# Performance work log

Hardware: AMD Instinct MI355X
Metric: run time of the kernel (lower is better)

Reference implementation:

```python
import jax, jax.numpy as jnp
import numpy as np
from jax import lax
from jax.scipy.special import logsumexp

B, T, L, K = 4, 512, 96, 64  # batch, sample_size, num_label, segment_max_len
W = K - 1                    # number of non-zero-start segment lengths considered
NEG = -1e30


def setup_inputs() -> dict:
    key = jax.random.key(0)
    k1, k2 = jax.random.split(key)
    segment_score = jax.random.normal(k1, (B, T, T, L), dtype=jnp.float32)
    transitions = jax.random.uniform(k2, (L + 1, L), dtype=jnp.float32)  # row L = BOS
    return {"segment_score": segment_score, "transitions": transitions}


def _log_z(segment_score, transitions):
    dtype = segment_score.dtype
    trans = transitions[:L]   # [Lp, Lc]
    bos = transitions[L]      # [Lc]
    # NOTE: original code stores exp(...) (not log) for frame 0 -- preserved faithfully.
    alpha0 = jnp.zeros((B, T, L), dtype)
    alpha0 = alpha0.at[:, 0, :].set(jnp.exp(segment_score[:, 0, 0, :] + bos[None, :]))

    w = jnp.arange(1, W + 1, dtype=dtype)  # weight (j+1) per window slot
    jidx = jnp.arange(W)

    def step(alpha, t):
        # scores of all segments ending at frame t: [B, T(start), L]
        seg_t = lax.dynamic_slice(segment_score, (0, 0, t, 0), (B, T, 1, L))[:, :, 0, :]
        base = jnp.maximum(t - W, 0)
        m = jnp.minimum(t, W)  # number of valid non-zero-start entries
        # window slot j: start frame = base+1+j, prev alpha frame = base+j, weight = j+1
        seg_win = lax.dynamic_slice(seg_t, (0, base + 1, 0), (B, W, L))      # [B,W,Lc]
        alpha_win = lax.dynamic_slice(alpha, (0, base, 0), (B, W, L))        # [B,W,Lp]
        total = (alpha_win[:, :, :, None]
                 + (seg_win * w[None, :, None])[:, :, None, :]
                 + (trans[None, :, :] * w[:, None, None])[None, :, :, :])    # [B,W,Lp,Lc]
        total = jnp.where(jidx[None, :, None, None] < m, total, NEG)
        # zero-start segment (only when t+1 <= K i.e. t <= W)
        tlen = (t + 1).astype(dtype)
        z = seg_t[:, 0, :] * tlen + bos[None, :] * tlen                       # [B,Lc]
        z = jnp.where(t <= W, z, NEG)
        cat = jnp.concatenate([total.reshape(B, W * L, L), z[:, None, :]], axis=1)
        new = logsumexp(cat, axis=1)                                          # [B,Lc]
        alpha = lax.dynamic_update_slice(alpha, new[:, None, :], (0, t, 0))
        return alpha, None

    alpha, _ = lax.scan(step, alpha0, jnp.arange(1, T))
    return logsumexp(alpha[:, T - 1, :], axis=1)  # [B]


def reference(segment_score, transitions):
    return _log_z(segment_score, transitions)
```

## Files before the change

### kernel.cpp

```cpp
#include <hip/hip_runtime.h>


#define Tn 512
#define Ln 96
#define HL 48
#define LSQ (Ln * Ln)
#define Wn 63
#define KCH 8
#define NROLE 32
#define NEGINF (-1e30f)
#define SENT 0x7FC00000u

#define AGENT __HIP_MEMORY_SCOPE_AGENT
#define WG __HIP_MEMORY_SCOPE_WORKGROUP
#define RLX __ATOMIC_RELAXED
#define LDSF() asm volatile("s_waitcnt lgkmcnt(0)" ::: "memory")
#define CBAR() asm volatile("" ::: "memory")
#define SIDX(b, i, t) ((((size_t)(b) * Tn + (i)) * Tn + (t)) * Ln)

typedef unsigned long long u64;
typedef unsigned int u32;
typedef unsigned short u16;

__device__ __forceinline__ float wsumred(float v) {
#pragma unroll
  for (int m = 32; m >= 1; m >>= 1) v += __shfl_xor(v, m, 64);
  return v;
}
__device__ __forceinline__ u64 pack2(float lo, float hi) {
  return (u64)__float_as_uint(lo) | ((u64)__float_as_uint(hi) << 32);
}
__device__ __forceinline__ u16 tobf16(float x) {
  return (u16)((__float_as_uint(x) + 0x8000u) >> 16);
}
__device__ __forceinline__ float wavemax48(float v) {
  int x;
  x = __builtin_amdgcn_update_dpp(__float_as_int(v), __float_as_int(v), 0xB1,
                                  0xF, 0xF, false);
  v = fmaxf(v, __int_as_float(x));
  x = __builtin_amdgcn_update_dpp(__float_as_int(v), __float_as_int(v), 0x4E,
                                  0xF, 0xF, false);
  v = fmaxf(v, __int_as_float(x));
  x = __builtin_amdgcn_update_dpp(__float_as_int(v), __float_as_int(v), 0x141,
                                  0xF, 0xF, false);
  v = fmaxf(v, __int_as_float(x));
  x = __builtin_amdgcn_update_dpp(__float_as_int(v), __float_as_int(v), 0x140,
                                  0xF, 0xF, false);
  v = fmaxf(v, __int_as_float(x));
  float r0 = __int_as_float(__builtin_amdgcn_readlane(__float_as_int(v), 0));
  float r1 = __int_as_float(__builtin_amdgcn_readlane(__float_as_int(v), 16));
  float r2 = __int_as_float(__builtin_amdgcn_readlane(__float_as_int(v), 32));
  float r3 = __int_as_float(__builtin_amdgcn_readlane(__float_as_int(v), 48));
  return fmaxf(fmaxf(r0, r1), fmaxf(r2, r3));
}
__device__ __forceinline__ float comb(float Slo, float Shi, float C0, float C1,
                                      float wseg) {
  const float Cm = fmaxf(C0, C1);
  return Cm + wseg + __logf(__expf(C0 - Cm) * Slo + __expf(C1 - Cm) * Shi);
}

#define MV1(SRC, RR, SLO, SHI)                                       \
  float SLO, SHI;                                                    \
  {                                                                  \
    const float4* A4 = (const float4*)(SRC);                         \
    float a0 = 0, a1 = 0, a2 = 0, a3 = 0;                            \
    _Pragma("unroll") for (int q = 0; q < 12; ++q) {                 \
      float4 a = A4[q];                                              \
      a0 = fmaf(a.x, RR[4 * q + 0], a0);                             \
      a1 = fmaf(a.y, RR[4 * q + 1], a1);                             \
      a2 = fmaf(a.z, RR[4 * q + 2], a2);                             \
      a3 = fmaf(a.w, RR[4 * q + 3], a3);                             \
    }                                                                \
    SLO = (a0 + a1) + (a2 + a3);                                     \
    float b0 = 0, b1 = 0, b2 = 0, b3 = 0;                            \
    _Pragma("unroll") for (int q = 12; q < 24; ++q) {                \
      float4 a = A4[q];                                              \
      b0 = fmaf(a.x, RR[4 * q + 0], b0);                             \
      b1 = fmaf(a.y, RR[4 * q + 1], b1);                             \
      b2 = fmaf(a.z, RR[4 * q + 2], b2);                             \
      b3 = fmaf(a.w, RR[4 * q + 3], b3);                             \
    }                                                                \
    SHI = (b0 + b1) + (b2 + b3);                                     \
  }

#define MVB(SRC, RR, SLO, SHI)                                               \
  float SLO, SHI;                                                            \
  {                                                                          \
    const uint4* A4 = (const uint4*)(SRC);                                   \
    float a0 = 0, a1 = 0, a2 = 0, a3 = 0;                                    \
    _Pragma("unroll") for (int q = 0; q < 6; ++q) {                          \
      uint4 a = A4[q];                                                       \
      a0 = fmaf(__uint_as_float(a.x << 16), RR[8 * q + 0], a0);              \
      a1 = fmaf(__uint_as_float(a.x & 0xFFFF0000u), RR[8 * q + 1], a1);      \
      a2 = fmaf(__uint_as_float(a.y << 16), RR[8 * q + 2], a2);              \
      a3 = fmaf(__uint_as_float(a.y & 0xFFFF0000u), RR[8 * q + 3], a3);      \
      a0 = fmaf(__uint_as_float(a.z << 16), RR[8 * q + 4], a0);              \
      a1 = fmaf(__uint_as_float(a.z & 0xFFFF0000u), RR[8 * q + 5], a1);      \
      a2 = fmaf(__uint_as_float(a.w << 16), RR[8 * q + 6], a2);              \
      a3 = fmaf(__uint_as_float(a.w & 0xFFFF0000u), RR[8 * q + 7], a3);      \
    }                                                                        \
    SLO = (a0 + a1) + (a2 + a3);                                             \
    float b0 = 0, b1 = 0, b2 = 0, b3 = 0;                                    \
    _Pragma("unroll") for (int q = 6; q < 12; ++q) {                         \
      uint4 a = A4[q];                                                       \
      b0 = fmaf(__uint_as_float(a.x << 16), RR[8 * q + 0], b0);              \
      b1 = fmaf(__uint_as_float(a.x & 0xFFFF0000u), RR[8 * q + 1], b1);      \
      b2 = fmaf(__uint_as_float(a.y << 16), RR[8 * q + 2], b2);              \
      b3 = fmaf(__uint_as_float(a.y & 0xFFFF0000u), RR[8 * q + 3], b3);      \
      b0 = fmaf(__uint_as_float(a.z << 16), RR[8 * q + 4], b0);              \
      b1 = fmaf(__uint_as_float(a.z & 0xFFFF0000u), RR[8 * q + 5], b1);      \
      b2 = fmaf(__uint_as_float(a.w << 16), RR[8 * q + 6], b2);              \
      b3 = fmaf(__uint_as_float(a.w & 0xFFFF0000u), RR[8 * q + 7], b3);      \
    }                                                                        \
    SHI = (b0 + b1) + (b2 + b3);                                             \
  }

__global__ void init_ws(u64* ws) {
  const size_t n1 = (size_t)4 * Tn * Ln;
  const size_t n = n1 * 9;
  for (size_t i = (size_t)blockIdx.x * blockDim.x + threadIdx.x; i < n;
       i += (size_t)gridDim.x * blockDim.x)
    ws[i] = (i < n1) ? (((u64)SENT) << 32) : 0ull;
}

__global__ __launch_bounds__(512, 1) void semicrf(
    const float* __restrict__ seg, const float* __restrict__ tr,
    float* __restrict__ out, u64* axp, u64* acc) {
  const int b = blockIdx.x / NROLE;
  const int role = blockIdx.x % NROLE;
  const int tid = threadIdx.x;

  __shared__ __align__(16) float E[LSQ];
  __shared__ __align__(16) u16 AlbRh[8][Ln];
  __shared__ float CRng[8][2];
  __shared__ float RESTm[4][Ln];
  __shared__ float RESTv[4][Ln];
  __shared__ __align__(16) float Alb_s[4][2][Ln];
  __shared__ float CstS[4][2][2];
  __shared__ float redbuf[2];
  __shared__ int seqA[2], rq[2][2], rfl[2];
  __shared__ int stg[4][2];

  if (tid < 2) { seqA[tid] = -1; rfl[tid] = -1; }
  if (tid < 4) rq[tid >> 1][tid & 1] = -1;
  if (tid < 8) stg[tid >> 1][tid & 1] = -1;
  for (int i = tid; i < LSQ; i += 512) E[i] = __expf(tr[i]);
  __syncthreads();

  if (role != 0) {
    const int pair = tid >> 7;
    const int tp = tid & 127;
    const int wv = tp >> 6;
    const int rl = tp & 63;
    const bool act = rl < HL;
    const int lab = wv * HL + (act ? rl : HL - 1);
    const int pu = (role - 1) * 4 + pair;
    const int d = 2 + (pu >> 1);
    const int par = pu & 1;
    const int j = d & 7;
    u64* chain = acc + (size_t)(j * 4 + b) * Tn * Ln;
    const u64* axB = axp + (size_t)b * Tn * Ln;
    float R[Ln];
#pragma unroll
    for (int lp = 0; lp < Ln; ++lp) R[lp] = E[lp * Ln + lab];
    int wc = 1;
    const bool aHead = (d + KCH > Wn);
    const int t0 = d + (((d ^ par) & 1) ? 1 : 0);

    for (int t = t0; t < Tn; t += 2) {
      const int s = t - d;
      const int w = (t <= Wn) ? (s + 1) : (64 - d);
      while (w > wc) {
        ++wc;
#pragma unroll
        for (int lp = 0; lp < Ln; ++lp) R[lp] *= E[lp * Ln + lab];
      }
      const float segv = seg[SIDX(b, s + 1, t) + lab];
      const size_t tIdx = (size_t)t * Ln + lab;
      const bool head = aHead || (s < KCH);
      u64 ua = 0;
      if (!head) ua = __hip_atomic_load(&chain[tIdx], RLX, AGENT);

      u64 up = __hip_atomic_load(&axB[(size_t)s * Ln + lab], RLX, AGENT);
      while ((u32)(up >> 32) == SENT)
        up = __hip_atomic_load(&axB[(size_t)s * Ln + lab], RLX, AGENT);

      const int buf = (t >> 1) & 1;
      if (act) Alb_s[pair][buf][lab] = __uint_as_float((u32)up);
      if (rl == 0) CstS[pair][buf][wv] = __uint_as_float((u32)(up >> 32));
      LDSF();
      __hip_atomic_store(&stg[pair][wv], t, RLX, WG);
      while (__hip_atomic_load(&stg[pair][wv ^ 1], RLX, WG) < t) {}
      CBAR();
      const float C0 = CstS[pair][buf][0], C1 = CstS[pair][buf][1];
      MV1(Alb_s[pair][buf], R, Slo, Shi)
      const float c = comb(Slo, Shi, C0, C1, (float)w * segv);

      float m, v;
      if (head) {
        m = c;
        v = 1.f;
      } else {
        while (((ua >> 32) & 0xFFu) != (u32)(d + KCH))
          ua = __hip_atomic_load(&chain[tIdx], RLX, AGENT);
        const float pm = __uint_as_float((u32)ua);
        const float pv = __uint_as_float(((u32)(ua >> 32)) & ~0xFFu);
        const float nm = fmaxf(pm, c);
        v = pv * __expf(pm - nm) + __expf(c - nm);
        m = nm;
      }
      if (act) {
        const u32 vb = (__float_as_uint(v) & ~0xFFu) | (u32)d;
        __hip_atomic_store(&chain[tIdx],
                           (u64)__float_as_uint(m) | ((u64)vb << 32), RLX,
                           AGENT);
      }
    }
    return;
  }

  const int w6 = tid >> 6;
  const int l = tid & 63;
  const bool act = l < HL;
  if (w6 >= 6) return;

  if (w6 < 2) {
    const int h = w6;
    const int lab = h * HL + (act ? l : HL - 1);
    u64* axpB = axp + (size_t)b * Tn * Ln;
    float R1[Ln];
#pragma unroll
    for (int lp = 0; lp < Ln; ++lp) R1[lp] = E[lp * Ln + lab];
    int w1c = 1;
    {
      const float bos = tr[LSQ + lab];
      const float a0 = __expf(seg[SIDX(b, 0, 0) + lab] + bos);
      const float Cw = wavemax48(act ? a0 : NEGINF);
      const float ax0 = __expf(a0 - Cw);
      if (act) __hip_atomic_store(&axpB[lab], pack2(ax0, Cw), RLX, AGENT);
      if (act) AlbRh[0][lab] = tobf16(ax0);
      if (l == 0) CRng[0][h] = Cw;
      LDSF();
      __hip_atomic_store(&seqA[h], 0, RLX, WG);
    }
    float s1q0 = seg[SIDX(b, 1, 1) + lab];
    float s1q1 = seg[SIDX(b, 2, 2) + lab];

    for (int t = 1; t < Tn; ++t) {
      const int s = t - 1;
      const float s1 = s1q0;
      s1q0 = s1q1;
      if (t + 2 < Tn) s1q1 = seg[SIDX(b, t + 2, t + 2) + lab];
      const int w1 = (t <= Wn) ? t : Wn;
      if (w1 > w1c) {
        w1c = w1;
#pragma unroll
        for (int lp = 0; lp < Ln; ++lp) R1[lp] *= E[lp * Ln + lab];
      }
      while (__hip_atomic_load(&seqA[h ^ 1], RLX, WG) < s) {}
      CBAR();
      const float C0 = CRng[s & 7][0], C1 = CRng[s & 7][1];
      MVB(AlbRh[s & 7], R1, Slo, Shi)
      const float c1 = comb(Slo, Shi, C0, C1, (float)w1 * s1);
      while (__hip_atomic_load(&rq[t & 1][h], RLX, WG) < t) {}
      CBAR();
      const float mr = RESTm[t & 3][lab], vr = RESTv[t & 3][lab];
      const float M = fmaxf(c1, mr);
      const float vs = __expf(c1 - M) + vr * __expf(mr - M);
      const float alpha = M + __logf(vs);
      const float Cw = wavemax48(act ? alpha : NEGINF);
      const float axn = __expf(alpha - Cw);
      if (act)
        __hip_atomic_store(&axpB[(size_t)t * Ln + lab], pack2(axn, Cw), RLX,
                           AGENT);
      if (act) AlbRh[t & 7][lab] = tobf16(axn);
      if (l == 0) CRng[t & 7][h] = Cw;
      LDSF();
      __hip_atomic_store(&seqA[h], t, RLX, WG);
      if (t == Tn - 1) {
        const float sm = wsumred(act ? axn : 0.f);
        const float Gw = Cw + __logf(sm);
        if (l == 0) redbuf[h] = Gw;
        LDSF();
        __hip_atomic_store(&rfl[h], 1, RLX, WG);
        if (h == 0 && l == 0) {
          while (__hip_atomic_load(&rfl[1], RLX, WG) < 1) {}
          CBAR();
          const float G0 = redbuf[0], G1 = redbuf[1];
          const float Mx = fmaxf(G0, G1);
          out[b] = Mx + __logf(__expf(G0 - Mx) + __expf(G1 - Mx));
        }
      }
    }
    return;
  }

  {
    const int p = (w6 - 2) >> 1;
    const int h = (w6 - 2) & 1;
    const int lab = h * HL + (act ? l : HL - 1);
    const float bos = tr[LSQ + lab];
    const int endd[8] = {8, 9, 2, 3, 4, 5, 6, 7};
    const int t0 = (p == 1) ? 1 : 2;
    float zq0 = (t0 <= Wn) ? seg[SIDX(b, 0, t0) + lab] : 0.f;
    float zq1 = (t0 + 2 <= Wn) ? seg[SIDX(b, 0, t0 + 2) + lab] : 0.f;
    u64 u[8];
#pragma unroll
    for (int jj = 0; jj < 8; ++jj) {
      u[jj] = 0;
      if (jj != 2 && jj != 3 && t0 >= endd[jj])
        u[jj] = __hip_atomic_load(
            &acc[(((size_t)jj * 4 + b) * Tn + t0) * Ln + lab], RLX, AGENT);
    }

    for (int t = t0; t < Tn; t += 2) {
      if (t >= 2)
        u[2] = __hip_atomic_load(
            &acc[(((size_t)2 * 4 + b) * Tn + t) * Ln + lab], RLX, AGENT);
      if (t >= 3)
        u[3] = __hip_atomic_load(
            &acc[(((size_t)3 * 4 + b) * Tn + t) * Ln + lab], RLX, AGENT);
      const float szv = zq0;
      zq0 = zq1;
      if (t + 4 <= Wn) zq1 = seg[SIDX(b, 0, t + 4) + lab];

      const float zv = (t <= Wn) ? (float)(t + 1) * (szv + bos) : NEGINF;
      float M = zv;
      float em[8], ev[8];
#pragma unroll
      for (int jj = 0; jj < 8; ++jj) {
        if (jj == 2 || jj == 3) continue;
        if (t >= endd[jj]) {
          const size_t aIdx = (((size_t)jj * 4 + b) * Tn + t) * Ln + lab;
          while (((u[jj] >> 32) & 0xFFu) != (u32)endd[jj])
            u[jj] = __hip_atomic_load(&acc[aIdx], RLX, AGENT);
          em[jj] = __uint_as_float((u32)u[jj]);
          ev[jj] = __uint_as_float(((u32)(u[jj] >> 32)) & ~0xFFu);
          M = fmaxf(M, em[jj]);
        } else {
          em[jj] = NEGINF;
          ev[jj] = 0.f;
        }
      }
#pragma unroll
      for (int jj = 2; jj <= 3; ++jj) {
        if (t >= endd[jj]) {
          const size_t aIdx = (((size_t)jj * 4 + b) * Tn + t) * Ln + lab;
          while (((u[jj] >> 32) & 0xFFu) != (u32)endd[jj])
            u[jj] = __hip_atomic_load(&acc[aIdx], RLX, AGENT);
          em[jj] = __uint_as_float((u32)u[jj]);
          ev[jj] = __uint_as_float(((u32)(u[jj] >> 32)) & ~0xFFu);
          M = fmaxf(M, em[jj]);
        } else {
          em[jj] = NEGINF;
          ev[jj] = 0.f;
        }
      }
      float vs = __expf(zv - M);
#pragma unroll
      for (int jj = 0; jj < 8; ++jj) vs += ev[jj] * __expf(em[jj] - M);

      if (act) {
        RESTm[t & 3][lab] = M;
        RESTv[t & 3][lab] = vs;
      }
      LDSF();
      __hip_atomic_store(&rq[p][h], t, RLX, WG);

      const int tn = t + 2;
      if (tn < Tn) {
#pragma unroll
        for (int jj = 0; jj < 8; ++jj)
          if (jj != 2 && jj != 3 && tn >= endd[jj])
            u[jj] = __hip_atomic_load(
                &acc[(((size_t)jj * 4 + b) * Tn + tn) * Ln + lab], RLX, AGENT);
      }
    }
    return;
  }
}

extern "C" void kernel_launch(void* const* d_in, const int* in_sizes, int n_in,
                              void* d_out, int out_size, void* d_ws,
                              size_t ws_size, hipStream_t stream) {
  const float* seg = (const float*)d_in[0];
  const float* tr = (const float*)d_in[1];
  float* out = (float*)d_out;

  u64* axp = (u64*)d_ws;
  u64* acc = axp + (size_t)4 * Tn * Ln;

  hipLaunchKernelGGL(init_ws, dim3(2048), dim3(256), 0, stream, (u64*)d_ws);
  hipLaunchKernelGGL(semicrf, dim3(4 * NROLE), dim3(512), 0, stream, seg, tr,
                     out, axp, acc);
}
```

Baseline: 862.0 us.

## Compute segment lengths 2-3 in role-0 block with s_barrier lockstep sync

Moves the computation of segment lengths 2 and 3 (d=2,3) from the remote chain blocks into the role-0 block, where dedicated waves write them to LDS slots for the alpha waves to combine directly. The per-wave LDS flag spinning is replaced with workgroup s_barrier lockstep across all eight waves. The remote workers are regrouped to cover d>=4 with a stride-3 time schedule, and NROLE rises to 46. This aims to shorten the critical serial path through global atomics for the short lengths. In exchange it adds barrier overhead on every step and relies on all waves staying in lockstep.

New measurement: 757.2 us. -12.2%, faster.

```diff
diff --git a/kernel.cpp b/kernel.cpp
--- a/kernel.cpp
+++ b/kernel.cpp
@@ -7,7 +7,7 @@
 #define LSQ (Ln * Ln)
 #define Wn 63
 #define KCH 8
-#define NROLE 32
+#define NROLE 46
 #define NEGINF (-1e30f)
 #define SENT 0x7FC00000u
 
@@ -16,6 +16,13 @@
 #define RLX __ATOMIC_RELAXED
 #define LDSF() asm volatile("s_waitcnt lgkmcnt(0)" ::: "memory")
 #define CBAR() asm volatile("" ::: "memory")
+#define BARRIER()                 \
+  do {                            \
+    LDSF();                       \
+    CBAR();                       \
+    __builtin_amdgcn_s_barrier(); \
+    CBAR();                       \
+  } while (0)
 #define SIDX(b, i, t) ((((size_t)(b) * Tn + (i)) * Tn + (t)) * Ln)
 
 typedef unsigned long long u64;
@@ -133,16 +140,15 @@
   __shared__ __align__(16) float E[LSQ];
   __shared__ __align__(16) u16 AlbRh[8][Ln];
   __shared__ float CRng[8][2];
+  __shared__ __align__(16) float slotC2[4][Ln];
+  __shared__ __align__(16) float slotC3[4][Ln];
   __shared__ float RESTm[4][Ln];
   __shared__ float RESTv[4][Ln];
   __shared__ __align__(16) float Alb_s[4][2][Ln];
   __shared__ float CstS[4][2][2];
   __shared__ float redbuf[2];
-  __shared__ int seqA[2], rq[2][2], rfl[2];
   __shared__ int stg[4][2];
 
-  if (tid < 2) { seqA[tid] = -1; rfl[tid] = -1; }
-  if (tid < 4) rq[tid >> 1][tid & 1] = -1;
   if (tid < 8) stg[tid >> 1][tid & 1] = -1;
   for (int i = tid; i < LSQ; i += 512) E[i] = __expf(tr[i]);
   __syncthreads();
@@ -155,8 +161,8 @@
     const bool act = rl < HL;
     const int lab = wv * HL + (act ? rl : HL - 1);
     const int pu = (role - 1) * 4 + pair;
-    const int d = 2 + (pu >> 1);
-    const int par = pu & 1;
+    const int d = 4 + pu / 3;
+    const int m3 = pu % 3;
     const int j = d & 7;
     u64* chain = acc + (size_t)(j * 4 + b) * Tn * Ln;
     const u64* axB = axp + (size_t)b * Tn * Ln;
@@ -165,9 +171,10 @@
     for (int lp = 0; lp < Ln; ++lp) R[lp] = E[lp * Ln + lab];
     int wc = 1;
     const bool aHead = (d + KCH > Wn);
-    const int t0 = d + (((d ^ par) & 1) ? 1 : 0);
-
-    for (int t = t0; t < Tn; t += 2) {
+    const int t0 = d + ((m3 - (d % 3)) + 3) % 3;
+    int bufi = 0;
+
+    for (int t = t0; t < Tn; t += 3) {
       const int s = t - d;
       const int w = (t <= Wn) ? (s + 1) : (64 - d);
       while (w > wc) {
@@ -185,16 +192,16 @@
       while ((u32)(up >> 32) == SENT)
         up = __hip_atomic_load(&axB[(size_t)s * Ln + lab], RLX, AGENT);
 
-      const int buf = (t >> 1) & 1;
-      if (act) Alb_s[pair][buf][lab] = __uint_as_float((u32)up);
-      if (rl == 0) CstS[pair][buf][wv] = __uint_as_float((u32)(up >> 32));
+      if (act) Alb_s[pair][bufi][lab] = __uint_as_float((u32)up);
+      if (rl == 0) CstS[pair][bufi][wv] = __uint_as_float((u32)(up >> 32));
       LDSF();
       __hip_atomic_store(&stg[pair][wv], t, RLX, WG);
       while (__hip_atomic_load(&stg[pair][wv ^ 1], RLX, WG) < t) {}
       CBAR();
-      const float C0 = CstS[pair][buf][0], C1 = CstS[pair][buf][1];
-      MV1(Alb_s[pair][buf], R, Slo, Shi)
+      const float C0 = CstS[pair][bufi][0], C1 = CstS[pair][bufi][1];
+      MV1(Alb_s[pair][bufi], R, Slo, Shi)
       const float c = comb(Slo, Shi, C0, C1, (float)w * segv);
+      bufi ^= 1;
 
       float m, v;
       if (head) {
@@ -222,51 +229,48 @@
   const int w6 = tid >> 6;
   const int l = tid & 63;
   const bool act = l < HL;
-  if (w6 >= 6) return;
+  const int h = w6 & 1;
+  const int lab = h * HL + (act ? l : HL - 1);
+  u64* axpB = axp + (size_t)b * Tn * Ln;
+  const float bos = tr[LSQ + lab];
 
   if (w6 < 2) {
-    const int h = w6;
-    const int lab = h * HL + (act ? l : HL - 1);
-    u64* axpB = axp + (size_t)b * Tn * Ln;
     float R1[Ln];
 #pragma unroll
     for (int lp = 0; lp < Ln; ++lp) R1[lp] = E[lp * Ln + lab];
     int w1c = 1;
+    float q0 = seg[SIDX(b, 1, 1) + lab];
+    float q1 = seg[SIDX(b, 2, 2) + lab];
     {
-      const float bos = tr[LSQ + lab];
       const float a0 = __expf(seg[SIDX(b, 0, 0) + lab] + bos);
       const float Cw = wavemax48(act ? a0 : NEGINF);
       const float ax0 = __expf(a0 - Cw);
       if (act) __hip_atomic_store(&axpB[lab], pack2(ax0, Cw), RLX, AGENT);
       if (act) AlbRh[0][lab] = tobf16(ax0);
       if (l == 0) CRng[0][h] = Cw;
-      LDSF();
-      __hip_atomic_store(&seqA[h], 0, RLX, WG);
-    }
-    float s1q0 = seg[SIDX(b, 1, 1) + lab];
-    float s1q1 = seg[SIDX(b, 2, 2) + lab];
-
+    }
+    BARRIER();
+
+    float lastAx = 0.f, lastCw = 0.f;
     for (int t = 1; t < Tn; ++t) {
-      const int s = t - 1;
-      const float s1 = s1q0;
-      s1q0 = s1q1;
-      if (t + 2 < Tn) s1q1 = seg[SIDX(b, t + 2, t + 2) + lab];
+      const float s1 = q0;
+      q0 = q1;
+      if (t + 2 < Tn) q1 = seg[SIDX(b, t + 2, t + 2) + lab];
       const int w1 = (t <= Wn) ? t : Wn;
       if (w1 > w1c) {
         w1c = w1;
 #pragma unroll
         for (int lp = 0; lp < Ln; ++lp) R1[lp] *= E[lp * Ln + lab];
       }
-      while (__hip_atomic_load(&seqA[h ^ 1], RLX, WG) < s) {}
-      CBAR();
-      const float C0 = CRng[s & 7][0], C1 = CRng[s & 7][1];
-      MVB(AlbRh[s & 7], R1, Slo, Shi)
+      const float C0 = CRng[(t - 1) & 7][0], C1 = CRng[(t - 1) & 7][1];
+      MVB(AlbRh[(t - 1) & 7], R1, Slo, Shi)
       const float c1 = comb(Slo, Shi, C0, C1, (float)w1 * s1);
-      while (__hip_atomic_load(&rq[t & 1][h], RLX, WG) < t) {}
-      CBAR();
+      const float c2 = (t >= 2) ? slotC2[t & 3][lab] : NEGINF;
+      const float c3 = (t >= 3) ? slotC3[t & 3][lab] : NEGINF;
       const float mr = RESTm[t & 3][lab], vr = RESTv[t & 3][lab];
-      const float M = fmaxf(c1, mr);
-      const float vs = __expf(c1 - M) + vr * __expf(mr - M);
+      const float M = fmaxf(fmaxf(c1, c2), fmaxf(c3, mr));
+      const float vs = __expf(c1 - M) + __expf(c2 - M) + __expf(c3 - M) +
+                       vr * __expf(mr - M);
       const float alpha = M + __logf(vs);
       const float Cw = wavemax48(act ? alpha : NEGINF);
       const float axn = __expf(alpha - Cw);
@@ -275,107 +279,154 @@
                            AGENT);
       if (act) AlbRh[t & 7][lab] = tobf16(axn);
       if (l == 0) CRng[t & 7][h] = Cw;
-      LDSF();
-      __hip_atomic_store(&seqA[h], t, RLX, WG);
-      if (t == Tn - 1) {
-        const float sm = wsumred(act ? axn : 0.f);
-        const float Gw = Cw + __logf(sm);
-        if (l == 0) redbuf[h] = Gw;
-        LDSF();
-        __hip_atomic_store(&rfl[h], 1, RLX, WG);
-        if (h == 0 && l == 0) {
-          while (__hip_atomic_load(&rfl[1], RLX, WG) < 1) {}
-          CBAR();
-          const float G0 = redbuf[0], G1 = redbuf[1];
-          const float Mx = fmaxf(G0, G1);
-          out[b] = Mx + __logf(__expf(G0 - Mx) + __expf(G1 - Mx));
+      lastAx = axn;
+      lastCw = Cw;
+      BARRIER();
+    }
+    const float sm = wsumred(act ? lastAx : 0.f);
+    if (l == 0) redbuf[h] = lastCw + __logf(sm);
+    BARRIER();
+    if (w6 == 0 && l == 0) {
+      const float G0 = redbuf[0], G1 = redbuf[1];
+      const float Mx = fmaxf(G0, G1);
+      out[b] = Mx + __logf(__expf(G0 - Mx) + __expf(G1 - Mx));
+    }
+    return;
+  }
+
+  if (w6 < 4) {
+    float R2[Ln];
+#pragma unroll
+    for (int lp = 0; lp < Ln; ++lp) R2[lp] = E[lp * Ln + lab];
+    int wc = 1;
+    float q0 = seg[SIDX(b, 1, 2) + lab];
+    float q1 = seg[SIDX(b, 2, 3) + lab];
+    BARRIER();
+    for (int t = 1; t < Tn; ++t) {
+      const int tp1 = t + 1;
+      if (tp1 < Tn) {
+        const float sv = q0;
+        q0 = q1;
+        if (tp1 + 2 < Tn) q1 = seg[SIDX(b, tp1 + 1, tp1 + 2) + lab];
+        const int w = (tp1 <= Wn) ? (tp1 - 1) : 62;
+        if (w > wc) {
+          wc = w;
+#pragma unroll
+          for (int lp = 0; lp < Ln; ++lp) R2[lp] *= E[lp * Ln + lab];
         }
-      }
-    }
+        const float C0 = CRng[(t - 1) & 7][0], C1 = CRng[(t - 1) & 7][1];
+        MVB(AlbRh[(t - 1) & 7], R2, Slo, Shi)
+        const float c = comb(Slo, Shi, C0, C1, (float)w * sv);
+        if (act) slotC2[tp1 & 3][lab] = c;
+      }
+      BARRIER();
+    }
+    BARRIER();
     return;
   }
 
+  if (w6 < 6) {
+    float R3[Ln];
+#pragma unroll
+    for (int lp = 0; lp < Ln; ++lp) R3[lp] = E[lp * Ln + lab];
+    int wc = 1;
+    float q0 = 0.f;
+    float q1 = seg[SIDX(b, 1, 3) + lab];
+    BARRIER();
+    for (int t = 1; t < Tn; ++t) {
+      const int tp1 = t + 1;
+      if (tp1 < Tn) {
+        const float sv = q0;
+        q0 = q1;
+        if (tp1 + 2 < Tn) q1 = seg[SIDX(b, tp1, tp1 + 2) + lab];
+        if (tp1 >= 3) {
+          const int w = (tp1 <= Wn) ? (tp1 - 2) : 61;
+          if (w > wc) {
+            wc = w;
+#pragma unroll
+            for (int lp = 0; lp < Ln; ++lp) R3[lp] *= E[lp * Ln + lab];
+          }
+          const float C0 = CRng[(t - 2) & 7][0], C1 = CRng[(t - 2) & 7][1];
+          MVB(AlbRh[(t - 2) & 7], R3, Slo, Shi)
+          const float c = comb(Slo, Shi, C0, C1, (float)w * sv);
+          if (act) slotC3[tp1 & 3][lab] = c;
+        }
+      }
+      BARRIER();
+    }
+    BARRIER();
+    return;
+  }
+
   {
-    const int p = (w6 - 2) >> 1;
-    const int h = (w6 - 2) & 1;
-    const int lab = h * HL + (act ? l : HL - 1);
-    const float bos = tr[LSQ + lab];
-    const int endd[8] = {8, 9, 2, 3, 4, 5, 6, 7};
-    const int t0 = (p == 1) ? 1 : 2;
-    float zq0 = (t0 <= Wn) ? seg[SIDX(b, 0, t0) + lab] : 0.f;
-    float zq1 = (t0 + 2 <= Wn) ? seg[SIDX(b, 0, t0 + 2) + lab] : 0.f;
-    u64 u[8];
+    const int endd[8] = {8, 9, 10, 11, 4, 5, 6, 7};
+    u64 UA[8], UB[8];
 #pragma unroll
     for (int jj = 0; jj < 8; ++jj) {
-      u[jj] = 0;
-      if (jj != 2 && jj != 3 && t0 >= endd[jj])
-        u[jj] = __hip_atomic_load(
-            &acc[(((size_t)jj * 4 + b) * Tn + t0) * Ln + lab], RLX, AGENT);
-    }
-
-    for (int t = t0; t < Tn; t += 2) {
-      if (t >= 2)
-        u[2] = __hip_atomic_load(
-            &acc[(((size_t)2 * 4 + b) * Tn + t) * Ln + lab], RLX, AGENT);
-      if (t >= 3)
-        u[3] = __hip_atomic_load(
-            &acc[(((size_t)3 * 4 + b) * Tn + t) * Ln + lab], RLX, AGENT);
-      const float szv = zq0;
-      zq0 = zq1;
-      if (t + 4 <= Wn) zq1 = seg[SIDX(b, 0, t + 4) + lab];
-
-      const float zv = (t <= Wn) ? (float)(t + 1) * (szv + bos) : NEGINF;
-      float M = zv;
-      float em[8], ev[8];
-#pragma unroll
-      for (int jj = 0; jj < 8; ++jj) {
-        if (jj == 2 || jj == 3) continue;
-        if (t >= endd[jj]) {
-          const size_t aIdx = (((size_t)jj * 4 + b) * Tn + t) * Ln + lab;
-          while (((u[jj] >> 32) & 0xFFu) != (u32)endd[jj])
-            u[jj] = __hip_atomic_load(&acc[aIdx], RLX, AGENT);
-          em[jj] = __uint_as_float((u32)u[jj]);
-          ev[jj] = __uint_as_float(((u32)(u[jj] >> 32)) & ~0xFFu);
-          M = fmaxf(M, em[jj]);
+      UA[jj] = 0;
+      UB[jj] = 0;
+    }
+    float zq0 = seg[SIDX(b, 0, 2) + lab];
+    float zq1 = seg[SIDX(b, 0, 3) + lab];
+    {
+      const float zv = 2.f * (seg[SIDX(b, 0, 1) + lab] + bos);
+      if (act) {
+        RESTm[1][lab] = zv;
+        RESTv[1][lab] = 1.f;
+      }
+    }
+    BARRIER();
+
+#define RESTSTEP(U)                                                          \
+  {                                                                          \
+    float M = zv;                                                            \
+    float em[8], ev[8];                                                      \
+    _Pragma("unroll") for (int jj = 0; jj < 8; ++jj) {                       \
+      if (tp1 >= endd[jj]) {                                                 \
+        const size_t aIdx = (((size_t)jj * 4 + b) * Tn + tp1) * Ln + lab;    \
+        while (((U[jj] >> 32) & 0xFFu) != (u32)endd[jj])                     \
+          U[jj] = __hip_atomic_load(&acc[aIdx], RLX, AGENT);                 \
+        em[jj] = __uint_as_float((u32)U[jj]);                                \
+        ev[jj] = __uint_as_float(((u32)(U[jj] >> 32)) & ~0xFFu);             \
+        M = fmaxf(M, em[jj]);                                                \
+      } else {                                                               \
+        em[jj] = NEGINF;                                                     \
+        ev[jj] = 0.f;                                                        \
+      }                                                                      \
+    }                                                                        \
+    float vs = __expf(zv - M);                                               \
+    _Pragma("unroll") for (int jj = 0; jj < 8; ++jj) vs +=                   \
+        ev[jj] * __expf(em[jj] - M);                                         \
+    if (act) {                                                               \
+      RESTm[tp1 & 3][lab] = M;                                               \
+      RESTv[tp1 & 3][lab] = vs;                                              \
+    }                                                                        \
+    if (tp1 + 2 < Tn) {                                                      \
+      _Pragma("unroll") for (int jj = 0; jj < 8; ++jj) {                     \
+        if (tp1 + 2 >= endd[jj])                                             \
+          U[jj] = __hip_atomic_load(                                         \
+              &acc[(((size_t)jj * 4 + b) * Tn + (tp1 + 2)) * Ln + lab], RLX, \
+              AGENT);                                                        \
+      }                                                                      \
+    }                                                                        \
+  }
+
+    for (int t = 1; t < Tn; ++t) {
+      const int tp1 = t + 1;
+      if (tp1 < Tn) {
+        const float zv =
+            (tp1 <= Wn) ? (float)(tp1 + 1) * (zq0 + bos) : NEGINF;
+        zq0 = zq1;
+        if (tp1 + 2 <= Wn) zq1 = seg[SIDX(b, 0, tp1 + 2) + lab];
+        if (tp1 & 1) {
+          RESTSTEP(UA)
         } else {
-          em[jj] = NEGINF;
-          ev[jj] = 0.f;
+          RESTSTEP(UB)
         }
       }
-#pragma unroll
-      for (int jj = 2; jj <= 3; ++jj) {
-        if (t >= endd[jj]) {
-          const size_t aIdx = (((size_t)jj * 4 + b) * Tn + t) * Ln + lab;
-          while (((u[jj] >> 32) & 0xFFu) != (u32)endd[jj])
-            u[jj] = __hip_atomic_load(&acc[aIdx], RLX, AGENT);
-          em[jj] = __uint_as_float((u32)u[jj]);
-          ev[jj] = __uint_as_float(((u32)(u[jj] >> 32)) & ~0xFFu);
-          M = fmaxf(M, em[jj]);
-        } else {
-          em[jj] = NEGINF;
-          ev[jj] = 0.f;
-        }
-      }
-      float vs = __expf(zv - M);
-#pragma unroll
-      for (int jj = 0; jj < 8; ++jj) vs += ev[jj] * __expf(em[jj] - M);
-
-      if (act) {
-        RESTm[t & 3][lab] = M;
-        RESTv[t & 3][lab] = vs;
-      }
-      LDSF();
-      __hip_atomic_store(&rq[p][h], t, RLX, WG);
-
-      const int tn = t + 2;
-      if (tn < Tn) {
-#pragma unroll
-        for (int jj = 0; jj < 8; ++jj)
-          if (jj != 2 && jj != 3 && tn >= endd[jj])
-            u[jj] = __hip_atomic_load(
-                &acc[(((size_t)jj * 4 + b) * Tn + tn) * Ln + lab], RLX, AGENT);
-      }
-    }
+      BARRIER();
+    }
+    BARRIER();
     return;
   }
 }
```
